# Kernel optimization log

Hardware: AMD Instinct MI355X
Metric: run time of the kernel (lower is better)

Reference implementation:

```python
import jax, jax.numpy as jnp
import numpy as np
import math

VOCAB = 50257
EMBED = 256
RES = 2048
SQV = int(math.ceil(math.sqrt(VOCAB)))  # 225
B, T = 4, 512


def setup_inputs() -> dict:
    key = jax.random.key(0)
    ks = jax.random.split(key, 10)
    idx = jax.random.randint(ks[0], (B, T), 0, VOCAB)
    targets = jax.random.randint(ks[1], (B, T), 0, VOCAB)
    wte = 0.02 * jax.random.normal(ks[2], (VOCAB, EMBED), dtype=jnp.float32)
    W_in = jax.random.uniform(ks[3], (RES, EMBED), minval=-0.1, maxval=0.1, dtype=jnp.float32)
    W_ih = jax.random.uniform(ks[4], (RES, RES), minval=-1.0, maxval=1.0, dtype=jnp.float32)
    # approximate spectral-radius rescale: sr(uniform(-1,1) NxN) ~ sqrt(N/3)
    sr_scale = 0.99 / float(np.sqrt(RES / 3.0))
    W_hh = sr_scale * jax.random.uniform(ks[5], (RES, RES), minval=-1.0, maxval=1.0, dtype=jnp.float32)
    b_ih = jax.random.uniform(ks[6], (RES,), minval=-0.1, maxval=0.1, dtype=jnp.float32)
    b_hh = jax.random.uniform(ks[7], (RES,), minval=-0.1, maxval=0.1, dtype=jnp.float32)
    Wh1 = (1.0 / np.sqrt(RES)) * jax.random.normal(ks[8], (SQV, RES), dtype=jnp.float32)
    Wh2 = (1.0 / np.sqrt(RES)) * jax.random.normal(ks[9], (SQV, RES), dtype=jnp.float32)
    return {"idx": idx, "targets": targets, "wte": wte, "W_in": W_in,
            "W_ih": W_ih, "b_ih": b_ih, "W_hh": W_hh, "b_hh": b_hh,
            "Wh1": Wh1, "Wh2": Wh2}


def _esn_states(idx, wte, W_in, W_ih, b_ih, W_hh, b_hh):
    emb = wte[idx]                                  # [B,T,E]
    proj = jnp.einsum('bte,re->btr', emb, W_in)     # [B,T,R]
    xin = jnp.einsum('btr,sr->bts', proj, W_ih) + b_ih  # precompute input part
    h0 = jnp.zeros((idx.shape[0], RES), dtype=proj.dtype)

    def step(h, xt):  # xt: [B,R]
        h = jnp.tanh(xt + h @ W_hh.T + b_hh)
        return h, h

    h_n, states = jax.lax.scan(step, h0, jnp.swapaxes(xin, 0, 1))  # states [T,B,R]
    return jnp.swapaxes(states, 0, 1), h_n


def reference(idx, targets, wte, W_in, W_ih, b_ih, W_hh, b_hh, Wh1, Wh2):
    states, h_n = _esn_states(idx, wte, W_in, W_ih, b_ih, W_hh, b_hh)  # [B,T,R]
    logits1 = jnp.einsum('btr,vr->btv', states, Wh1)  # [B,T,SQV]
    logits2 = jnp.einsum('btr,vr->btv', states, Wh2)

    # masked dual cross-entropy (ignore -1)
    mask = (targets != -1)
    safe_t = jnp.where(mask, targets, 0)
    t_row = safe_t // SQV
    t_col = safe_t % SQV
    lp1 = jax.nn.log_softmax(logits1, axis=-1)
    lp2 = jax.nn.log_softmax(logits2, axis=-1)
    nll1 = -jnp.take_along_axis(lp1, t_row[..., None], axis=-1)[..., 0]
    nll2 = -jnp.take_along_axis(lp2, t_col[..., None], axis=-1)[..., 0]
    cnt = jnp.maximum(mask.sum(), 1)
    loss = (jnp.where(mask, nll1, 0.0).sum() + jnp.where(mask, nll2, 0.0).sum()) / cnt

    # combined log-probs -> logits over full vocab
    combined = lp1[..., :, None] + lp2[..., None, :]          # [B,T,SQV,SQV]
    logits = combined.reshape(idx.shape[0], idx.shape[1], SQV * SQV)[:, :, :VOCAB]
    return logits, loss, h_n[None]  # h_n [1,B,R] like torch RNN
```

## Files before the change

kernel.cpp:

```cpp
#include <hip/hip_runtime.h>
#include <stdint.h>
#include <math.h>

#define R_  2048
#define E_  256
#define T_  512
#define BT_ 2048
#define SQ_ 225
#define V_  50257
#define NWG_R 128

typedef float f32x4 __attribute__((ext_vector_type(4)));

__global__ __launch_bounds__(256) void k_gemm_mt(const float* __restrict__ Win,
                                                 const float* __restrict__ Wih,
                                                 float* __restrict__ Mt) {
  __shared__ __align__(16) float As[32][68];
  __shared__ __align__(16) float Bs[32][68];
  const int m0 = blockIdx.x * 64;
  const int n0 = blockIdx.y * 64;
  const int tid = threadIdx.x;
  const int tx = tid & 15, ty = tid >> 4;
  float acc[4][4] = {};
  for (int k0 = 0; k0 < R_; k0 += 32) {
    {
      int mm = tid & 63, kk = tid >> 6;
#pragma unroll
      for (int u = 0; u < 8; ++u)
        As[kk + u * 4][mm] = Win[(size_t)(k0 + kk + u * 4) * E_ + m0 + mm];
    }
    {
      int kk = tid & 31, nn = tid >> 5;
#pragma unroll
      for (int u = 0; u < 8; ++u)
        Bs[kk][nn + u * 8] = Wih[(size_t)(n0 + nn + u * 8) * R_ + k0 + kk];
    }
    __syncthreads();
#pragma unroll
    for (int kk = 0; kk < 32; ++kk) {
      float4 a = *(const float4*)&As[kk][ty * 4];
      float4 b = *(const float4*)&Bs[kk][tx * 4];
      acc[0][0] += a.x * b.x; acc[0][1] += a.x * b.y; acc[0][2] += a.x * b.z; acc[0][3] += a.x * b.w;
      acc[1][0] += a.y * b.x; acc[1][1] += a.y * b.y; acc[1][2] += a.y * b.z; acc[1][3] += a.y * b.w;
      acc[2][0] += a.z * b.x; acc[2][1] += a.z * b.y; acc[2][2] += a.z * b.z; acc[2][3] += a.z * b.w;
      acc[3][0] += a.w * b.x; acc[3][1] += a.w * b.y; acc[3][2] += a.w * b.z; acc[3][3] += a.w * b.w;
    }
    __syncthreads();
  }
#pragma unroll
  for (int i = 0; i < 4; ++i) {
    float4 v = make_float4(acc[i][0], acc[i][1], acc[i][2], acc[i][3]);
    *(float4*)&Mt[(size_t)(m0 + ty * 4 + i) * R_ + n0 + tx * 4] = v;
  }
}

__global__ __launch_bounds__(256) void k_xin(const int* __restrict__ idx,
                                             const float* __restrict__ wte,
                                             const float* __restrict__ Mt,
                                             const float* __restrict__ bih,
                                             float* __restrict__ xinT) {
  __shared__ __align__(16) float As[32][68];
  __shared__ __align__(16) float Bs[32][68];
  __shared__ __align__(16) float Ts[64][68];
  __shared__ int rowL[64];
  const int m0 = blockIdx.x * 64;
  const int n0 = blockIdx.y * 64;
  const int tid = threadIdx.x;
  const int tx = tid & 15, ty = tid >> 4;
  if (tid < 64) rowL[tid] = idx[m0 + tid];
  __syncthreads();
  float acc[4][4] = {};
  for (int k0 = 0; k0 < E_; k0 += 32) {
    {
      int kk = tid & 31, mm = tid >> 5;
#pragma unroll
      for (int u = 0; u < 8; ++u)
        As[kk][mm + u * 8] = wte[(size_t)rowL[mm + u * 8] * E_ + k0 + kk];
    }
    {
      int nn = tid & 63, kk = tid >> 6;
#pragma unroll
      for (int u = 0; u < 8; ++u)
        Bs[kk + u * 4][nn] = Mt[(size_t)(k0 + kk + u * 4) * R_ + n0 + nn];
    }
    __syncthreads();
#pragma unroll
    for (int kk = 0; kk < 32; ++kk) {
      float4 a = *(const float4*)&As[kk][ty * 4];
      float4 b = *(const float4*)&Bs[kk][tx * 4];
      acc[0][0] += a.x * b.x; acc[0][1] += a.x * b.y; acc[0][2] += a.x * b.z; acc[0][3] += a.x * b.w;
      acc[1][0] += a.y * b.x; acc[1][1] += a.y * b.y; acc[1][2] += a.y * b.z; acc[1][3] += a.y * b.w;
      acc[2][0] += a.z * b.x; acc[2][1] += a.z * b.y; acc[2][2] += a.z * b.z; acc[2][3] += a.z * b.w;
      acc[3][0] += a.w * b.x; acc[3][1] += a.w * b.y; acc[3][2] += a.w * b.z; acc[3][3] += a.w * b.w;
    }
    __syncthreads();
  }
  float4 bv = *(const float4*)&bih[n0 + tx * 4];
#pragma unroll
  for (int i = 0; i < 4; ++i) {
    Ts[tx * 4 + 0][ty * 4 + i] = acc[i][0] + bv.x;
    Ts[tx * 4 + 1][ty * 4 + i] = acc[i][1] + bv.y;
    Ts[tx * 4 + 2][ty * 4 + i] = acc[i][2] + bv.z;
    Ts[tx * 4 + 3][ty * 4 + i] = acc[i][3] + bv.w;
  }
  __syncthreads();
  {
    int nn = tid >> 2, qq = tid & 3;
#pragma unroll
    for (int u = 0; u < 4; ++u) {
      float4 v = *(const float4*)&Ts[nn][(qq + u * 4) * 4];
      *(float4*)&xinT[(size_t)(n0 + nn) * BT_ + m0 + (qq + u * 4) * 4] = v;
    }
  }
}

__global__ __launch_bounds__(256, 1) void k_recur(const float* __restrict__ Whh,
                                                  const float* __restrict__ xinT,
                                                  const float* __restrict__ bhh_g,
                                                  float* hg,
                                                  float* __restrict__ stT,
                                                  unsigned* flags) {
  __shared__ __align__(16) float hL[4][R_];
  __shared__ float stS[2][8][72];
  const int tid = threadIdx.x;
  const int w = tid >> 6;
  const int c = tid & 63;
  const int row0 = blockIdx.x * 16 + w * 4;

  float W[4][32];
#pragma unroll
  for (int i = 0; i < 4; ++i) {
    const float* src = Whh + (size_t)(row0 + i) * R_;
#pragma unroll
    for (int k = 0; k < 8; ++k) {
      float4 v = *(const float4*)(src + k * 256 + c * 4);
      W[i][k * 4 + 0] = v.x; W[i][k * 4 + 1] = v.y; W[i][k * 4 + 2] = v.z; W[i][k * 4 + 3] = v.w;
    }
  }
  const int li = c >> 2, lb = c & 3;
  float bhl = (c < 16) ? bhh_g[row0 + li] : 0.f;
  const int fr = tid >> 3, flb = (tid >> 1) & 3, fth = tid & 1;

  for (int t = 0; t < T_; ++t) {
    const int p = t & 1;
    float xvl = 0.f;
    if (c < 16) xvl = xinT[(size_t)(row0 + li) * BT_ + lb * T_ + t];

    if (t) {
      const unsigned* f0 = flags + (size_t)c * 16;
      const unsigned* f1 = flags + (size_t)(c + 64) * 16;
      long g = 0;
      while (__hip_atomic_load(f0, __ATOMIC_RELAXED, __HIP_MEMORY_SCOPE_AGENT) < (unsigned)t ||
             __hip_atomic_load(f1, __ATOMIC_RELAXED, __HIP_MEMORY_SCOPE_AGENT) < (unsigned)t) {
        __builtin_amdgcn_s_sleep(1);
        if (++g > (1L << 24)) break;
      }
    }

    {
      const f32x4* hsrc = (const f32x4*)(hg + (size_t)p * 8192);
      f32x4 tmp[8];
#pragma unroll
      for (int j = 0; j < 8; ++j) {
        const f32x4* ap = hsrc + tid + j * 256;
        asm volatile("global_load_dwordx4 %0, %1, off sc0 sc1" : "=&v"(tmp[j]) : "v"(ap));
      }
      asm volatile("s_waitcnt vmcnt(0)" ::: "memory");
      __builtin_amdgcn_sched_barrier(0);
      f32x4* hLv = (f32x4*)hL;
#pragma unroll
      for (int j = 0; j < 8; ++j) hLv[tid + j * 256] = tmp[j];
    }
    __syncthreads();

    float acc[4][4] = {};
#pragma unroll
    for (int k = 0; k < 8; ++k) {
      float4 h4[4];
#pragma unroll
      for (int b = 0; b < 4; ++b) h4[b] = *(const float4*)&hL[b][k * 256 + c * 4];
#pragma unroll
      for (int i = 0; i < 4; ++i) {
#pragma unroll
        for (int b = 0; b < 4; ++b) {
          acc[i][b] += W[i][k * 4 + 0] * h4[b].x + W[i][k * 4 + 1] * h4[b].y
                     + W[i][k * 4 + 2] * h4[b].z + W[i][k * 4 + 3] * h4[b].w;
        }
      }
    }
#pragma unroll
    for (int i = 0; i < 4; ++i)
#pragma unroll
      for (int b = 0; b < 4; ++b) {
        float v = acc[i][b];
        v += __shfl_xor(v, 32); v += __shfl_xor(v, 16); v += __shfl_xor(v, 8);
        v += __shfl_xor(v, 4);  v += __shfl_xor(v, 2);  v += __shfl_xor(v, 1);
        acc[i][b] = v;
      }
    if (c < 16) {
      float val = acc[0][0];
#pragma unroll
      for (int i = 0; i < 4; ++i)
#pragma unroll
        for (int b = 0; b < 4; ++b) {
          int k = i * 4 + b;
          if (k > 0) val = (c == k) ? acc[i][b] : val;
        }
      float hn = tanhf(xvl + val + bhl);
      __hip_atomic_store(&hg[(size_t)(1 - p) * 8192 + lb * R_ + row0 + li], hn,
                         __ATOMIC_RELAXED, __HIP_MEMORY_SCOPE_AGENT);
      stS[(t >> 3) & 1][t & 7][lb * 16 + w * 4 + li] = hn;
    }
    __syncthreads();
    if (tid == 0) {
      __hip_atomic_store(flags + (size_t)blockIdx.x * 16, (unsigned)(t + 1),
                         __ATOMIC_RELAXED, __HIP_MEMORY_SCOPE_AGENT);
    }
    if ((t & 7) == 7 && tid < 128) {
      const int buf = (t >> 3) & 1, t0 = t - 7;
      f32x4 v;
      v.x = stS[buf][fth * 4 + 0][flb * 16 + fr];
      v.y = stS[buf][fth * 4 + 1][flb * 16 + fr];
      v.z = stS[buf][fth * 4 + 2][flb * 16 + fr];
      v.w = stS[buf][fth * 4 + 3][flb * 16 + fr];
      *(f32x4*)&stT[(size_t)(blockIdx.x * 16 + fr) * BT_ + flb * T_ + t0 + fth * 4] = v;
    }
  }
}

__global__ __launch_bounds__(256) void k_logits(const float* __restrict__ stT,
                                                const float* __restrict__ Wh1,
                                                const float* __restrict__ Wh2,
                                                float* __restrict__ lg1,
                                                float* __restrict__ lg2) {
  __shared__ __align__(16) float As[32][68];
  __shared__ __align__(16) float Bs[32][68];
  const int m0 = blockIdx.x * 64;
  const int n0 = blockIdx.y * 64;
  const int tid = threadIdx.x;
  const int tx = tid & 15, ty = tid >> 4;
  float acc[4][4] = {};
  for (int k0 = 0; k0 < R_; k0 += 32) {
    {
      int mm = tid & 63, kk = tid >> 6;
#pragma unroll
      for (int u = 0; u < 8; ++u)
        As[kk + u * 4][mm] = stT[(size_t)(k0 + kk + u * 4) * BT_ + m0 + mm];
    }
    {
      int kk = tid & 31, nn = tid >> 5;
#pragma unroll
      for (int u = 0; u < 8; ++u) {
        int n = n0 + nn + u * 8;
        float v = 0.f;
        if (n < SQ_)            v = Wh1[(size_t)n * R_ + k0 + kk];
        else if (n < 2 * SQ_)   v = Wh2[(size_t)(n - SQ_) * R_ + k0 + kk];
        Bs[kk][nn + u * 8] = v;
      }
    }
    __syncthreads();
#pragma unroll
    for (int kk = 0; kk < 32; ++kk) {
      float4 a = *(const float4*)&As[kk][ty * 4];
      float4 b = *(const float4*)&Bs[kk][tx * 4];
      acc[0][0] += a.x * b.x; acc[0][1] += a.x * b.y; acc[0][2] += a.x * b.z; acc[0][3] += a.x * b.w;
      acc[1][0] += a.y * b.x; acc[1][1] += a.y * b.y; acc[1][2] += a.y * b.z; acc[1][3] += a.y * b.w;
      acc[2][0] += a.z * b.x; acc[2][1] += a.z * b.y; acc[2][2] += a.z * b.z; acc[2][3] += a.z * b.w;
      acc[3][0] += a.w * b.x; acc[3][1] += a.w * b.y; acc[3][2] += a.w * b.z; acc[3][3] += a.w * b.w;
    }
    __syncthreads();
  }
#pragma unroll
  for (int i = 0; i < 4; ++i)
#pragma unroll
    for (int j = 0; j < 4; ++j) {
      int n = n0 + tx * 4 + j;
      int m = m0 + ty * 4 + i;
      if (n < SQ_)          lg1[(size_t)m * 256 + n] = acc[i][j];
      else if (n < 2 * SQ_) lg2[(size_t)m * 256 + (n - SQ_)] = acc[i][j];
    }
}

__global__ __launch_bounds__(256) void k_lsm(float* lg1, float* lg2,
                                             const int* __restrict__ tgt, float* ctrl) {
  const int bt = blockIdx.x;
  const int head = blockIdx.y;
  float* lg = (head ? lg2 : lg1) + (size_t)bt * 256;
  const int tid = threadIdx.x;
  __shared__ float red[8];
  float x = (tid < SQ_) ? lg[tid] : -1e30f;
  float m = x;
#pragma unroll
  for (int o = 32; o >= 1; o >>= 1) m = fmaxf(m, __shfl_down(m, o));
  if ((tid & 63) == 0) red[tid >> 6] = m;
  __syncthreads();
  if (tid == 0) red[4] = fmaxf(fmaxf(red[0], red[1]), fmaxf(red[2], red[3]));
  __syncthreads();
  float mx = red[4];
  float e = (tid < SQ_) ? __expf(x - mx) : 0.f;
  float s = e;
#pragma unroll
  for (int o = 32; o >= 1; o >>= 1) s += __shfl_down(s, o);
  if ((tid & 63) == 0) red[tid >> 6] = s;
  __syncthreads();
  if (tid == 0) red[5] = logf(red[0] + red[1] + red[2] + red[3]);
  __syncthreads();
  float lp = x - mx - red[5];
  if (tid < SQ_) lg[tid] = lp;
  int t = tgt[bt];
  if (t != -1) {
    int trow = (int)(((uint64_t)(unsigned)t * 19088744ULL) >> 32);
    int tcol = t - trow * 225;
    int want = head ? tcol : trow;
    if (tid == want) atomicAdd(&ctrl[1], -lp);
    if (head == 0 && tid == 0) atomicAdd((int*)ctrl + 2, 1);
  }
}

__global__ __launch_bounds__(256) void k_write(const float* __restrict__ lg1,
                                               const float* __restrict__ lg2,
                                               float* __restrict__ out) {
  __shared__ float l1[SQ_], l2[SQ_];
  const int bt = blockIdx.x;
  const int tid = threadIdx.x;
  if (tid < SQ_) {
    l1[tid] = lg1[(size_t)bt * 256 + tid];
    l2[tid] = lg2[(size_t)bt * 256 + tid];
  }
  __syncthreads();
  const int vbase = blockIdx.y * 4096;
  float* o = out + (size_t)bt * V_;
#pragma unroll
  for (int i = 0; i < 16; ++i) {
    int v = vbase + i * 256 + tid;
    if (v < V_) {
      int row = (int)(((uint64_t)(unsigned)v * 19088744ULL) >> 32);
      int col = v - row * 225;
      o[v] = l1[row] + l2[col];
    }
  }
}

__global__ __launch_bounds__(256) void k_tail(const float* __restrict__ hg,
                                              const float* __restrict__ ctrl,
                                              float* __restrict__ out) {
  int i = blockIdx.x * 256 + threadIdx.x;
  if (i < 8192) {
    out[(size_t)BT_ * V_ + 1 + i] = hg[i];
  } else if (i == 8192) {
    int cnt = ((const int*)ctrl)[2];
    if (cnt < 1) cnt = 1;
    out[(size_t)BT_ * V_] = ctrl[1] / (float)cnt;
  }
}

extern "C" void kernel_launch(void* const* d_in, const int* in_sizes, int n_in,
                              void* d_out, int out_size, void* d_ws, size_t ws_size,
                              hipStream_t stream) {
  (void)in_sizes; (void)n_in; (void)out_size; (void)ws_size;
  const int*   idx = (const int*)d_in[0];
  const int*   tgt = (const int*)d_in[1];
  const float* wte = (const float*)d_in[2];
  const float* Win = (const float*)d_in[3];
  const float* Wih = (const float*)d_in[4];
  const float* bih = (const float*)d_in[5];
  const float* Whh = (const float*)d_in[6];
  const float* bhh = (const float*)d_in[7];
  const float* Wh1 = (const float*)d_in[8];
  const float* Wh2 = (const float*)d_in[9];

  float* ws    = (float*)d_ws;
  float* ctrl  = ws;
  unsigned* fl = (unsigned*)(ws + 64);
  float* hg    = ws + 64 + 2048;
  float* Mt    = hg + 16384;
  float* xinT  = Mt + (size_t)E_ * R_;
  float* stT   = xinT + (size_t)BT_ * R_;
  float* lg1   = xinT;
  float* lg2   = xinT + (size_t)BT_ * 256;
  float* out   = (float*)d_out;

  hipMemsetAsync(d_ws, 0, (64 + 2048 + 16384) * sizeof(float), stream);
  k_gemm_mt<<<dim3(E_ / 64, R_ / 64), 256, 0, stream>>>(Win, Wih, Mt);
  k_xin<<<dim3(BT_ / 64, R_ / 64), 256, 0, stream>>>(idx, wte, Mt, bih, xinT);
  k_recur<<<dim3(NWG_R), 256, 0, stream>>>(Whh, xinT, bhh, hg, stT, fl);
  k_logits<<<dim3(BT_ / 64, 8), 256, 0, stream>>>(stT, Wh1, Wh2, lg1, lg2);
  k_lsm<<<dim3(BT_, 2), 256, 0, stream>>>(lg1, lg2, tgt, ctrl);
  k_write<<<dim3(BT_, 13), 256, 0, stream>>>(lg1, lg2, out);
  k_tail<<<dim3(33), 256, 0, stream>>>(hg, ctrl, out);
}
```

Before: 3.448 ms.

## Halve recurrence workgroups to 64 with 512 threads and blocked hidden-state layout

The persistent recurrence kernel now uses 64 workgroups of 512 threads, each owning 32 rows, instead of 128 workgroups of 256 threads. Each waiting thread now polls one flag instead of two, which cuts the cross-workgroup barrier cost per timestep. The global hidden-state buffer is stored in a workgroup-blocked layout so each block writes contiguously, and the tail kernel un-permutes it when copying h_n out. In exchange the grid covers fewer CUs, and 512 threads each holding 128 weight registers raises register pressure and could cause spills.

```diff
diff --git a/kernel.cpp b/kernel.cpp
--- a/kernel.cpp
+++ b/kernel.cpp
@@ -8,7 +8,7 @@
 #define BT_ 2048
 #define SQ_ 225
 #define V_  50257
-#define NWG_R 128
+#define NWG_R 64
 
 typedef float f32x4 __attribute__((ext_vector_type(4)));
 
@@ -114,18 +114,18 @@
   }
 }
 
-__global__ __launch_bounds__(256, 1) void k_recur(const float* __restrict__ Whh,
+__global__ __launch_bounds__(512, 1) void k_recur(const float* __restrict__ Whh,
                                                   const float* __restrict__ xinT,
                                                   const float* __restrict__ bhh_g,
                                                   float* hg,
                                                   float* __restrict__ stT,
                                                   unsigned* flags) {
   __shared__ __align__(16) float hL[4][R_];
-  __shared__ float stS[2][8][72];
+  __shared__ float stS[2][8][136];
   const int tid = threadIdx.x;
   const int w = tid >> 6;
   const int c = tid & 63;
-  const int row0 = blockIdx.x * 16 + w * 4;
+  const int row0 = blockIdx.x * 32 + w * 4;
 
   float W[4][32];
 #pragma unroll
@@ -148,28 +148,31 @@
 
     if (t) {
       const unsigned* f0 = flags + (size_t)c * 16;
-      const unsigned* f1 = flags + (size_t)(c + 64) * 16;
       long g = 0;
-      while (__hip_atomic_load(f0, __ATOMIC_RELAXED, __HIP_MEMORY_SCOPE_AGENT) < (unsigned)t ||
-             __hip_atomic_load(f1, __ATOMIC_RELAXED, __HIP_MEMORY_SCOPE_AGENT) < (unsigned)t) {
+      while (__hip_atomic_load(f0, __ATOMIC_RELAXED, __HIP_MEMORY_SCOPE_AGENT) < (unsigned)t) {
         __builtin_amdgcn_s_sleep(1);
         if (++g > (1L << 24)) break;
       }
     }
 
-    {
-      const f32x4* hsrc = (const f32x4*)(hg + (size_t)p * 8192);
-      f32x4 tmp[8];
-#pragma unroll
-      for (int j = 0; j < 8; ++j) {
-        const f32x4* ap = hsrc + tid + j * 256;
+    f32x4 tmp[4];
+    {
+      const f32x4* base = (const f32x4*)(hg + (size_t)p * 8192);
+#pragma unroll
+      for (int j = 0; j < 4; ++j) {
+        const f32x4* ap = base + tid + j * 512;
         asm volatile("global_load_dwordx4 %0, %1, off sc0 sc1" : "=&v"(tmp[j]) : "v"(ap));
       }
       asm volatile("s_waitcnt vmcnt(0)" ::: "memory");
       __builtin_amdgcn_sched_barrier(0);
-      f32x4* hLv = (f32x4*)hL;
-#pragma unroll
-      for (int j = 0; j < 8; ++j) hLv[tid + j * 256] = tmp[j];
+    }
+#pragma unroll
+    for (int j = 0; j < 4; ++j) {
+      int q = tid + j * 512;
+      int wg = q >> 5;
+      int b  = (q >> 3) & 3;
+      int rl = (q & 7) << 2;
+      *(f32x4*)&hL[b][wg * 32 + rl] = tmp[j];
     }
     __syncthreads();
 
@@ -207,23 +210,24 @@
           if (k > 0) val = (c == k) ? acc[i][b] : val;
         }
       float hn = tanhf(xvl + val + bhl);
-      __hip_atomic_store(&hg[(size_t)(1 - p) * 8192 + lb * R_ + row0 + li], hn,
-                         __ATOMIC_RELAXED, __HIP_MEMORY_SCOPE_AGENT);
-      stS[(t >> 3) & 1][t & 7][lb * 16 + w * 4 + li] = hn;
+      __hip_atomic_store(&hg[(size_t)(1 - p) * 8192 + blockIdx.x * 128
+                             + lb * 32 + w * 4 + li],
+                         hn, __ATOMIC_RELAXED, __HIP_MEMORY_SCOPE_AGENT);
+      stS[(t >> 3) & 1][t & 7][lb * 32 + w * 4 + li] = hn;
     }
     __syncthreads();
     if (tid == 0) {
       __hip_atomic_store(flags + (size_t)blockIdx.x * 16, (unsigned)(t + 1),
                          __ATOMIC_RELAXED, __HIP_MEMORY_SCOPE_AGENT);
     }
-    if ((t & 7) == 7 && tid < 128) {
+    if ((t & 7) == 7 && tid < 256) {
       const int buf = (t >> 3) & 1, t0 = t - 7;
       f32x4 v;
-      v.x = stS[buf][fth * 4 + 0][flb * 16 + fr];
-      v.y = stS[buf][fth * 4 + 1][flb * 16 + fr];
-      v.z = stS[buf][fth * 4 + 2][flb * 16 + fr];
-      v.w = stS[buf][fth * 4 + 3][flb * 16 + fr];
-      *(f32x4*)&stT[(size_t)(blockIdx.x * 16 + fr) * BT_ + flb * T_ + t0 + fth * 4] = v;
+      v.x = stS[buf][fth * 4 + 0][flb * 32 + fr];
+      v.y = stS[buf][fth * 4 + 1][flb * 32 + fr];
+      v.z = stS[buf][fth * 4 + 2][flb * 32 + fr];
+      v.w = stS[buf][fth * 4 + 3][flb * 32 + fr];
+      *(f32x4*)&stT[(size_t)(blockIdx.x * 32 + fr) * BT_ + flb * T_ + t0 + fth * 4] = v;
     }
   }
 }
@@ -346,7 +350,9 @@
                                               float* __restrict__ out) {
   int i = blockIdx.x * 256 + threadIdx.x;
   if (i < 8192) {
-    out[(size_t)BT_ * V_ + 1 + i] = hg[i];
+    int lb = i >> 11, r = i & 2047;
+    int wg = r >> 5, rl = r & 31;
+    out[(size_t)BT_ * V_ + 1 + i] = hg[wg * 128 + lb * 32 + rl];
   } else if (i == 8192) {
     int cnt = ((const int*)ctrl)[2];
     if (cnt < 1) cnt = 1;
@@ -372,18 +378,18 @@
   float* ws    = (float*)d_ws;
   float* ctrl  = ws;
   unsigned* fl = (unsigned*)(ws + 64);
-  float* hg    = ws + 64 + 2048;
-  float* Mt    = hg + 16384;
+  float* hg    = ws + 64 + 1024;
+  float* Mt    = hg + 2 * 8192;
   float* xinT  = Mt + (size_t)E_ * R_;
   float* stT   = xinT + (size_t)BT_ * R_;
   float* lg1   = xinT;
   float* lg2   = xinT + (size_t)BT_ * 256;
   float* out   = (float*)d_out;
 
-  hipMemsetAsync(d_ws, 0, (64 + 2048 + 16384) * sizeof(float), stream);
+  hipMemsetAsync(d_ws, 0, (64 + 1024 + 2 * 8192) * sizeof(float), stream);
   k_gemm_mt<<<dim3(E_ / 64, R_ / 64), 256, 0, stream>>>(Win, Wih, Mt);
   k_xin<<<dim3(BT_ / 64, R_ / 64), 256, 0, stream>>>(idx, wte, Mt, bih, xinT);
-  k_recur<<<dim3(NWG_R), 256, 0, stream>>>(Whh, xinT, bhh, hg, stT, fl);
+  k_recur<<<dim3(NWG_R), 512, 0, stream>>>(Whh, xinT, bhh, hg, stT, fl);
   k_logits<<<dim3(BT_ / 64, 8), 256, 0, stream>>>(stT, Wh1, Wh2, lg1, lg2);
   k_lsm<<<dim3(BT_, 2), 256, 0, stream>>>(lg1, lg2, tgt, ctrl);
   k_write<<<dim3(BT_, 13), 256, 0, stream>>>(lg1, lg2, out);
```

Result: slower. 3.641 ms (+5.6%).

## Replace flag barrier in recurrence with sentinel-based dataflow sync over 4-slot ring

Applied to the files above, without the earlier changes.

The recurrence kernel no longer has each workgroup poll per-block step counters and stage h through LDS behind __syncthreads. Each wave now owns one batch element and reads h directly from a 4-slot global ring. It spins until no value equals a sentinel bit pattern, then re-poisons an old slot for reuse. Work is split across 512 workgroups of 4 rows each, with two workgroups per CU, to raise parallelism and shorten each step's critical path. The costs are redundant global reads of h by every wave, a dependency on all 512 workgroups being co-resident, and correctness resting on the sentinel never being a real tanh output.

```diff
diff --git a/kernel.cpp b/kernel.cpp
--- a/kernel.cpp
+++ b/kernel.cpp
@@ -8,7 +8,6 @@
 #define BT_ 2048
 #define SQ_ 225
 #define V_  50257
-#define NWG_R 128
 
 typedef float f32x4 __attribute__((ext_vector_type(4)));
 
@@ -114,18 +113,17 @@
   }
 }
 
-__global__ __launch_bounds__(256, 1) void k_recur(const float* __restrict__ Whh,
+__global__ __launch_bounds__(256, 2) void k_recur(const float* __restrict__ Whh,
                                                   const float* __restrict__ xinT,
                                                   const float* __restrict__ bhh_g,
                                                   float* hg,
-                                                  float* __restrict__ stT,
-                                                  unsigned* flags) {
-  __shared__ __align__(16) float hL[4][R_];
-  __shared__ float stS[2][8][72];
+                                                  float* __restrict__ stT) {
+  __shared__ float stS[4][2][4][12];
   const int tid = threadIdx.x;
   const int w = tid >> 6;
   const int c = tid & 63;
-  const int row0 = blockIdx.x * 16 + w * 4;
+  const int b = w;
+  const int row0 = blockIdx.x * 4;
 
   float W[4][32];
 #pragma unroll
@@ -137,93 +135,70 @@
       W[i][k * 4 + 0] = v.x; W[i][k * 4 + 1] = v.y; W[i][k * 4 + 2] = v.z; W[i][k * 4 + 3] = v.w;
     }
   }
-  const int li = c >> 2, lb = c & 3;
-  float bhl = (c < 16) ? bhh_g[row0 + li] : 0.f;
-  const int fr = tid >> 3, flb = (tid >> 1) & 3, fth = tid & 1;
-
+  float bh = (c < 4) ? bhh_g[row0 + c] : 0.f;
+
+  const unsigned SENT = 0x7F7F7F7Fu;
+  union { unsigned u; float f; } sc; sc.u = SENT;
+  const float sf = sc.f;
+
+  long gtot = 0;
   for (int t = 0; t < T_; ++t) {
-    const int p = t & 1;
-    float xvl = 0.f;
-    if (c < 16) xvl = xinT[(size_t)(row0 + li) * BT_ + lb * T_ + t];
-
-    if (t) {
-      const unsigned* f0 = flags + (size_t)c * 16;
-      const unsigned* f1 = flags + (size_t)(c + 64) * 16;
-      long g = 0;
-      while (__hip_atomic_load(f0, __ATOMIC_RELAXED, __HIP_MEMORY_SCOPE_AGENT) < (unsigned)t ||
-             __hip_atomic_load(f1, __ATOMIC_RELAXED, __HIP_MEMORY_SCOPE_AGENT) < (unsigned)t) {
-        __builtin_amdgcn_s_sleep(1);
-        if (++g > (1L << 24)) break;
+    const int rs = t & 3, ns = (t + 1) & 3, zs = (t + 3) & 3;
+    float xvl = (c < 4) ? xinT[(size_t)(row0 + c) * BT_ + b * T_ + t] : 0.f;
+
+    const float* base = hg + (size_t)rs * 8192 + b * 2048;
+    f32x4 tmp[8];
+#pragma unroll
+    for (int k = 0; k < 8; ++k) {
+      const f32x4* ap = (const f32x4*)(base + k * 256 + c * 4);
+      asm volatile("global_load_dwordx4 %0, %1, off sc0 sc1" : "=&v"(tmp[k]) : "v"(ap));
+    }
+    asm volatile("s_waitcnt vmcnt(0)" ::: "memory");
+    __builtin_amdgcn_sched_barrier(0);
+#pragma unroll
+    for (int k = 0; k < 8; ++k) {
+      while (__float_as_uint(tmp[k].x) == SENT || __float_as_uint(tmp[k].y) == SENT ||
+             __float_as_uint(tmp[k].z) == SENT || __float_as_uint(tmp[k].w) == SENT) {
+        if (++gtot > (1L << 22)) break;
+        const f32x4* ap = (const f32x4*)(base + k * 256 + c * 4);
+        asm volatile("global_load_dwordx4 %0, %1, off sc0 sc1" : "=&v"(tmp[k]) : "v"(ap));
+        asm volatile("s_waitcnt vmcnt(0)" ::: "memory");
+        __builtin_amdgcn_sched_barrier(0);
       }
     }
-
-    {
-      const f32x4* hsrc = (const f32x4*)(hg + (size_t)p * 8192);
-      f32x4 tmp[8];
-#pragma unroll
-      for (int j = 0; j < 8; ++j) {
-        const f32x4* ap = hsrc + tid + j * 256;
-        asm volatile("global_load_dwordx4 %0, %1, off sc0 sc1" : "=&v"(tmp[j]) : "v"(ap));
-      }
+    if (c < 4)
+      __hip_atomic_store(&hg[(size_t)zs * 8192 + b * 2048 + row0 + c], sf,
+                         __ATOMIC_RELAXED, __HIP_MEMORY_SCOPE_AGENT);
+
+    float a0 = 0.f, a1 = 0.f, a2 = 0.f, a3 = 0.f;
+#pragma unroll
+    for (int k = 0; k < 8; ++k) {
+      a0 += W[0][k*4+0]*tmp[k].x + W[0][k*4+1]*tmp[k].y + W[0][k*4+2]*tmp[k].z + W[0][k*4+3]*tmp[k].w;
+      a1 += W[1][k*4+0]*tmp[k].x + W[1][k*4+1]*tmp[k].y + W[1][k*4+2]*tmp[k].z + W[1][k*4+3]*tmp[k].w;
+      a2 += W[2][k*4+0]*tmp[k].x + W[2][k*4+1]*tmp[k].y + W[2][k*4+2]*tmp[k].z + W[2][k*4+3]*tmp[k].w;
+      a3 += W[3][k*4+0]*tmp[k].x + W[3][k*4+1]*tmp[k].y + W[3][k*4+2]*tmp[k].z + W[3][k*4+3]*tmp[k].w;
+    }
+#pragma unroll
+    for (int o = 32; o >= 1; o >>= 1) {
+      a0 += __shfl_xor(a0, o); a1 += __shfl_xor(a1, o);
+      a2 += __shfl_xor(a2, o); a3 += __shfl_xor(a3, o);
+    }
+    if (c < 4) {
+      float val = a0;
+      val = (c == 1) ? a1 : val;
+      val = (c == 2) ? a2 : val;
+      val = (c == 3) ? a3 : val;
+      float hn = tanhf(xvl + val + bh);
       asm volatile("s_waitcnt vmcnt(0)" ::: "memory");
-      __builtin_amdgcn_sched_barrier(0);
-      f32x4* hLv = (f32x4*)hL;
-#pragma unroll
-      for (int j = 0; j < 8; ++j) hLv[tid + j * 256] = tmp[j];
-    }
-    __syncthreads();
-
-    float acc[4][4] = {};
-#pragma unroll
-    for (int k = 0; k < 8; ++k) {
-      float4 h4[4];
-#pragma unroll
-      for (int b = 0; b < 4; ++b) h4[b] = *(const float4*)&hL[b][k * 256 + c * 4];
-#pragma unroll
-      for (int i = 0; i < 4; ++i) {
-#pragma unroll
-        for (int b = 0; b < 4; ++b) {
-          acc[i][b] += W[i][k * 4 + 0] * h4[b].x + W[i][k * 4 + 1] * h4[b].y
-                     + W[i][k * 4 + 2] * h4[b].z + W[i][k * 4 + 3] * h4[b].w;
-        }
-      }
-    }
-#pragma unroll
-    for (int i = 0; i < 4; ++i)
-#pragma unroll
-      for (int b = 0; b < 4; ++b) {
-        float v = acc[i][b];
-        v += __shfl_xor(v, 32); v += __shfl_xor(v, 16); v += __shfl_xor(v, 8);
-        v += __shfl_xor(v, 4);  v += __shfl_xor(v, 2);  v += __shfl_xor(v, 1);
-        acc[i][b] = v;
-      }
-    if (c < 16) {
-      float val = acc[0][0];
-#pragma unroll
-      for (int i = 0; i < 4; ++i)
-#pragma unroll
-        for (int b = 0; b < 4; ++b) {
-          int k = i * 4 + b;
-          if (k > 0) val = (c == k) ? acc[i][b] : val;
-        }
-      float hn = tanhf(xvl + val + bhl);
-      __hip_atomic_store(&hg[(size_t)(1 - p) * 8192 + lb * R_ + row0 + li], hn,
+      __hip_atomic_store(&hg[(size_t)ns * 8192 + b * 2048 + row0 + c], hn,
                          __ATOMIC_RELAXED, __HIP_MEMORY_SCOPE_AGENT);
-      stS[(t >> 3) & 1][t & 7][lb * 16 + w * 4 + li] = hn;
-    }
-    __syncthreads();
-    if (tid == 0) {
-      __hip_atomic_store(flags + (size_t)blockIdx.x * 16, (unsigned)(t + 1),
-                         __ATOMIC_RELAXED, __HIP_MEMORY_SCOPE_AGENT);
-    }
-    if ((t & 7) == 7 && tid < 128) {
+      stS[w][(t >> 3) & 1][c][t & 7] = hn;
+    }
+    if ((t & 7) == 7 && c < 8) {
       const int buf = (t >> 3) & 1, t0 = t - 7;
-      f32x4 v;
-      v.x = stS[buf][fth * 4 + 0][flb * 16 + fr];
-      v.y = stS[buf][fth * 4 + 1][flb * 16 + fr];
-      v.z = stS[buf][fth * 4 + 2][flb * 16 + fr];
-      v.w = stS[buf][fth * 4 + 3][flb * 16 + fr];
-      *(f32x4*)&stT[(size_t)(blockIdx.x * 16 + fr) * BT_ + flb * T_ + t0 + fth * 4] = v;
+      const int li = c >> 1, th = c & 1;
+      f32x4 v = *(const f32x4*)&stS[w][buf][li][th * 4];
+      *(f32x4*)&stT[(size_t)(row0 + li) * BT_ + b * T_ + t0 + th * 4] = v;
     }
   }
 }
@@ -369,21 +344,21 @@
   const float* Wh1 = (const float*)d_in[8];
   const float* Wh2 = (const float*)d_in[9];
 
-  float* ws    = (float*)d_ws;
-  float* ctrl  = ws;
-  unsigned* fl = (unsigned*)(ws + 64);
-  float* hg    = ws + 64 + 2048;
-  float* Mt    = hg + 16384;
-  float* xinT  = Mt + (size_t)E_ * R_;
-  float* stT   = xinT + (size_t)BT_ * R_;
-  float* lg1   = xinT;
-  float* lg2   = xinT + (size_t)BT_ * 256;
-  float* out   = (float*)d_out;
-
-  hipMemsetAsync(d_ws, 0, (64 + 2048 + 16384) * sizeof(float), stream);
+  float* ws   = (float*)d_ws;
+  float* ctrl = ws;
+  float* hg   = ws + 64;
+  float* Mt   = hg + 4 * 8192;
+  float* xinT = Mt + (size_t)E_ * R_;
+  float* stT  = xinT + (size_t)BT_ * R_;
+  float* lg1  = xinT;
+  float* lg2  = xinT + (size_t)BT_ * 256;
+  float* out  = (float*)d_out;
+
+  hipMemsetAsync(ws, 0, (64 + 8192) * sizeof(float), stream);
+  hipMemsetAsync(hg + 8192, 0x7F, 3 * 8192 * sizeof(float), stream);
   k_gemm_mt<<<dim3(E_ / 64, R_ / 64), 256, 0, stream>>>(Win, Wih, Mt);
   k_xin<<<dim3(BT_ / 64, R_ / 64), 256, 0, stream>>>(idx, wte, Mt, bih, xinT);
-  k_recur<<<dim3(NWG_R), 256, 0, stream>>>(Whh, xinT, bhh, hg, stT, fl);
+  k_recur<<<dim3(512), 256, 0, stream>>>(Whh, xinT, bhh, hg, stT);
   k_logits<<<dim3(BT_ / 64, 8), 256, 0, stream>>>(stT, Wh1, Wh2, lg1, lg2);
   k_lsm<<<dim3(BT_, 2), 256, 0, stream>>>(lg1, lg2, tgt, ctrl);
   k_write<<<dim3(BT_, 13), 256, 0, stream>>>(lg1, lg2, out);
```

Measured after the change: 6.434 ms. +86.6%, slower.
